# Kernel optimization log

Hardware: AMD Instinct MI355X
Metric: run time of the kernel (lower is better)

## Reference

```python
import jax, jax.numpy as jnp
import numpy as np

T, F, D = 16, 16, 512      # n_textures, n_features, texture resolution
N, L, H, W = 4, 4, 512, 512  # batch, n_layers, render H, render W


def setup_inputs() -> dict:
    key = jax.random.key(0)
    k1, k2, k3 = jax.random.split(key, 3)
    # grid_sample expects normalized coords in [-1, 1]
    uv_inputs = jax.random.uniform(k1, (N, 2 * L, H, W), jnp.float32) * 2.0 - 1.0
    mask_inputs = jax.random.randint(k2, (N, L, H, W), 0, T).astype(jnp.int32)
    data = jax.random.normal(k3, (T, F, D, D), jnp.float32) * 0.1
    return {"uv_inputs": uv_inputs, "mask_inputs": mask_inputs, "data": data}


def _sample_layer(data_flat, tid, u, v):
    # data_flat: [T*D*D, F]; tid,u,v: [N,H,W]
    # Faithful to torch grid_sample(bilinear, padding_mode='border', align_corners=False):
    # summing sample(data[t]) * (mask==t) over t == per-pixel gather from texture tid.
    ix = jnp.clip((u + 1.0) * (D * 0.5) - 0.5, 0.0, D - 1.0)  # border clip
    iy = jnp.clip((v + 1.0) * (D * 0.5) - 0.5, 0.0, D - 1.0)
    x0f = jnp.floor(ix)
    y0f = jnp.floor(iy)
    wx = (ix - x0f)[..., None]
    wy = (iy - y0f)[..., None]
    x0 = x0f.astype(jnp.int32)
    y0 = y0f.astype(jnp.int32)
    x1 = jnp.minimum(x0 + 1, D - 1)
    y1 = jnp.minimum(y0 + 1, D - 1)
    valid = ((tid >= 0) & (tid < T))[..., None]
    base = jnp.clip(tid, 0, T - 1).astype(jnp.int32) * (D * D)

    def g(y, x):  # gather corner texels -> [N,H,W,F]
        return jnp.take(data_flat, base + y * D + x, axis=0)

    out = (g(y0, x0) * (1.0 - wx) * (1.0 - wy)
           + g(y0, x1) * wx * (1.0 - wy)
           + g(y1, x0) * (1.0 - wx) * wy
           + g(y1, x1) * wx * wy)
    return out * valid.astype(out.dtype)


def reference(uv_inputs, mask_inputs, data):
    # [T,F,D,D] -> [T*D*D, F] so a single flat index gathers a full texel
    data_flat = jnp.transpose(data, (0, 2, 3, 1)).reshape(T * D * D, F)
    layers = []
    for l in range(L):  # small fixed layer count
        u = uv_inputs[:, 2 * l]       # grid[...,0] = x
        v = uv_inputs[:, 2 * l + 1]   # grid[...,1] = y
        tid = mask_inputs[:, l]
        sampled = _sample_layer(data_flat, tid, u, v)  # [N,H,W,F]
        layers.append(jnp.transpose(sampled, (0, 3, 1, 2)))  # [N,F,H,W]
    return jnp.concatenate(layers, axis=1)  # [N, L*F, H, W]
```

## Files before the change

kernel.cpp:

```cpp
#include <hip/hip_runtime.h>

constexpr int T_ = 16, F_ = 16, D_ = 512;
constexpr int N_ = 4, L_ = 4, H_ = 512, W_ = 512;
constexpr int HW_ = H_ * W_;
constexpr size_t DATA_ELEMS = (size_t)T_ * F_ * D_ * D_;
constexpr size_t PLANE = (size_t)D_ * D_;

constexpr size_t QTAB_BYTES = (size_t)T_ * D_ * D_ * 64;

__device__ unsigned g_smax_bits[T_ * F_];

typedef float vfloat4 __attribute__((ext_vector_type(4)));
typedef unsigned int vuint4 __attribute__((ext_vector_type(4)));

__global__ void zero_smax_kernel() { g_smax_bits[threadIdx.x] = 0u; }

__global__ __launch_bounds__(256) void max_pass_kernel(
    const float* __restrict__ data)
{
    const vfloat4* p = (const vfloat4*)data + (size_t)blockIdx.x * 8192 + threadIdx.x;
    float m = 0.0f;
    #pragma unroll
    for (int i = 0; i < 32; ++i) {
        vfloat4 v = __builtin_nontemporal_load(p + i * 256);
        m = fmaxf(m, fmaxf(fmaxf(fabsf(v.x), fabsf(v.y)),
                           fmaxf(fabsf(v.z), fabsf(v.w))));
    }
    #pragma unroll
    for (int k = 1; k < 64; k <<= 1) m = fmaxf(m, __shfl_xor(m, k));
    if ((threadIdx.x & 63) == 0)
        atomicMax(&g_smax_bits[blockIdx.x >> 3], __float_as_uint(m));
}

__global__ __launch_bounds__(256) void quad_pack_kernel(
    const float*   __restrict__ data,
    unsigned char* __restrict__ qtab)
{
    int bid = (blockIdx.x & 7) * 2048 + (blockIdx.x >> 3);

    __shared__ float enc[F_];
    int tid = threadIdx.x;
    int qblock = bid * 256;
    int t = qblock >> 18;
    if (tid < F_) {
        float m = __uint_as_float(g_smax_bits[t * F_ + tid]);
        enc[tid] = (m > 0.0f) ? 127.0f / m : 0.0f;
    }
    __syncthreads();

    int lane = tid & 63;
    int wid  = tid >> 6;
    int qbase = qblock + wid * 64;
    int dx = lane & 1, dy = (lane >> 1) & 1;
    int q0 = qbase + (lane >> 2);

    const float* dbase = data + (size_t)t * F_ * PLANE;
    unsigned out[4][4] = {};
    #pragma unroll
    for (int k = 0; k < 4; ++k) {
        int q = q0 + 16 * k;
        int x = q & (D_ - 1), y = (q >> 9) & (D_ - 1);
        int sx = min(x + dx, D_ - 1);
        int sy = min(y + dy, D_ - 1);
        size_t off = (size_t)sy * D_ + sx;
        #pragma unroll
        for (int f = 0; f < F_; ++f) {
            float val = dbase[f * PLANE + off];
            int i8 = __float2int_rn(fminf(fmaxf(val * enc[f], -127.0f), 127.0f));
            out[k][f >> 2] |= ((unsigned)i8 & 0xFFu) << (8 * (f & 3));
        }
    }
    unsigned char* wbase = qtab + (size_t)qbase * 64;
    #pragma unroll
    for (int k = 0; k < 4; ++k)
        *(vuint4*)(wbase + (size_t)(lane + 64 * k) * 16) =
            (vuint4){out[k][0], out[k][1], out[k][2], out[k][3]};
}

__global__ __launch_bounds__(256) void tex_sample_quad_kernel(
    const float*         __restrict__ uv,
    const int*           __restrict__ mask,
    const unsigned char* __restrict__ qtab,
    float*               __restrict__ out)
{
    __shared__ float dec[T_ * F_];
    dec[threadIdx.x] = __uint_as_float(g_smax_bits[threadIdx.x]) * (1.0f / 127.0f);
    __syncthreads();

    int idx = blockIdx.x * blockDim.x + threadIdx.x;
    int w = idx & (W_ - 1);
    int h = (idx >> 9) & (H_ - 1);
    int l = (idx >> 18) & (L_ - 1);
    int n = idx >> 20;
    int hw = h * W_ + w;

    float u  = __builtin_nontemporal_load(uv   + ((size_t)(n * 2 * L_ + 2 * l)    ) * HW_ + hw);
    float v  = __builtin_nontemporal_load(uv   + ((size_t)(n * 2 * L_ + 2 * l + 1)) * HW_ + hw);
    int  tid = __builtin_nontemporal_load(mask + ((size_t)(n * L_ + l)) * HW_ + hw);

    float ix = fminf(fmaxf((u + 1.0f) * (D_ * 0.5f) - 0.5f, 0.0f), (float)(D_ - 1));
    float iy = fminf(fmaxf((v + 1.0f) * (D_ * 0.5f) - 0.5f, 0.0f), (float)(D_ - 1));
    float x0f = floorf(ix), y0f = floorf(iy);
    float wx = ix - x0f, wy = iy - y0f;
    int x0 = (int)x0f, y0 = (int)y0f;

    float valid = (tid >= 0 && tid < T_) ? 1.0f : 0.0f;
    int t = min(max(tid, 0), T_ - 1);

    float w00 = (1.0f - wx) * (1.0f - wy) * valid;
    float w01 = wx * (1.0f - wy) * valid;
    float w10 = (1.0f - wx) * wy * valid;
    float w11 = wx * wy * valid;

    size_t e = ((size_t)t * D_ + y0) * D_ + x0;
    const vuint4* ep = (const vuint4*)(qtab + e * 64);
    vuint4 A = ep[0];
    vuint4 B = ep[1];
    vuint4 C = ep[2];
    vuint4 Dq = ep[3];

    const float* dp = &dec[t * F_];
    float* obase = out + ((size_t)(n * L_ + l) * F_) * HW_ + hw;
    #pragma unroll
    for (int q = 0; q < 4; ++q) {
        unsigned a = A[q], b = B[q], c = C[q], d = Dq[q];
        #pragma unroll
        for (int k = 0; k < 4; ++k) {
            int f = 4 * q + k;
            float r = (float)((signed char)(a >> (8 * k))) * w00
                    + (float)((signed char)(b >> (8 * k))) * w01
                    + (float)((signed char)(c >> (8 * k))) * w10
                    + (float)((signed char)(d >> (8 * k))) * w11;
            __builtin_nontemporal_store(r * dp[f], obase + (size_t)f * HW_);
        }
    }
}

__global__ __launch_bounds__(256) void tex_sample_kernel(
    const float* __restrict__ uv,
    const int*   __restrict__ mask,
    const float* __restrict__ data,
    float*       __restrict__ out)
{
    int idx = blockIdx.x * blockDim.x + threadIdx.x;
    int w = idx & (W_ - 1);
    int h = (idx >> 9) & (H_ - 1);
    int l = (idx >> 18) & (L_ - 1);
    int n = idx >> 20;
    int hw = h * W_ + w;

    float u  = uv[((size_t)(n * 2 * L_ + 2 * l)     ) * HW_ + hw];
    float v  = uv[((size_t)(n * 2 * L_ + 2 * l + 1)) * HW_ + hw];
    int  tid = mask[((size_t)(n * L_ + l)) * HW_ + hw];

    float ix = fminf(fmaxf((u + 1.0f) * (D_ * 0.5f) - 0.5f, 0.0f), (float)(D_ - 1));
    float iy = fminf(fmaxf((v + 1.0f) * (D_ * 0.5f) - 0.5f, 0.0f), (float)(D_ - 1));
    float x0f = floorf(ix), y0f = floorf(iy);
    float wx = ix - x0f, wy = iy - y0f;
    int x0 = (int)x0f, y0 = (int)y0f;
    int x1 = min(x0 + 1, D_ - 1);
    int y1 = min(y0 + 1, D_ - 1);

    float valid = (tid >= 0 && tid < T_) ? 1.0f : 0.0f;
    int t = min(max(tid, 0), T_ - 1);

    float w00 = (1.0f - wx) * (1.0f - wy) * valid;
    float w01 = wx * (1.0f - wy) * valid;
    float w10 = (1.0f - wx) * wy * valid;
    float w11 = wx * wy * valid;

    const float* dbase = data + (size_t)t * F_ * PLANE;
    int r0 = y0 * D_;
    int r1 = y1 * D_;
    float* obase = out + ((size_t)(n * L_ + l) * F_) * HW_ + hw;

    #pragma unroll
    for (int f = 0; f < F_; ++f) {
        const float* dp = dbase + (size_t)f * PLANE;
        float v00 = dp[r0 + x0];
        float v01 = dp[r0 + x1];
        float v10 = dp[r1 + x0];
        float v11 = dp[r1 + x1];
        obase[(size_t)f * HW_] = v00 * w00 + v01 * w01 + v10 * w10 + v11 * w11;
    }
}

extern "C" void kernel_launch(void* const* d_in, const int* in_sizes, int n_in,
                              void* d_out, int out_size, void* d_ws, size_t ws_size,
                              hipStream_t stream) {
    const float* uv   = (const float*)d_in[0];
    const int*   mask = (const int*)d_in[1];
    const float* data = (const float*)d_in[2];
    float* out = (float*)d_out;

    int total = N_ * L_ * H_ * W_;

    if (ws_size >= QTAB_BYTES) {
        unsigned char* qtab = (unsigned char*)d_ws;
        zero_smax_kernel<<<1, T_ * F_, 0, stream>>>();
        max_pass_kernel<<<2048, 256, 0, stream>>>(data);
        quad_pack_kernel<<<T_ * D_ * D_ / 256, 256, 0, stream>>>(data, qtab);
        tex_sample_quad_kernel<<<total / 256, 256, 0, stream>>>(uv, mask, qtab, out);
    } else {
        tex_sample_kernel<<<total / 256, 256, 0, stream>>>(uv, mask, data, out);
    }
}
```

Baseline: 748.1 us.

## Stage quantized texture rows in LDS to build quad table with coalesced loads

The quad-packing pre-pass now loads whole texture rows with coalesced float4 loads, quantizes them to int8 into shared memory (4 rows plus a halo row per block), then assembles the 2x2 neighbour quads from LDS. The old version loaded each texel four times with scattered scalar loads. The table layout also changes so each 16-byte group holds the four corners of one feature instead of one corner across four features, and the sampler is adjusted to match. The costs are about 41KB of LDS per block, which limits occupancy, and dropping the explicit clamp before rounding.

New measurement: 648.7 us. 13.3% less time.

```diff
diff --git a/kernel.cpp b/kernel.cpp
--- a/kernel.cpp
+++ b/kernel.cpp
@@ -32,49 +32,72 @@
         atomicMax(&g_smax_bits[blockIdx.x >> 3], __float_as_uint(m));
 }
 
-__global__ __launch_bounds__(256) void quad_pack_kernel(
+constexpr int QROWS = 4;
+constexpr int IROWS = QROWS + 1;
+constexpr int LDSP  = 520;
+
+__global__ __launch_bounds__(256) void quad_pack_kernel_v2(
     const float*   __restrict__ data,
     unsigned char* __restrict__ qtab)
 {
-    int bid = (blockIdx.x & 7) * 2048 + (blockIdx.x >> 3);
-
     __shared__ float enc[F_];
+    __shared__ unsigned char q8[F_][IROWS][LDSP];
+
+    int bid = blockIdx.x;
+    int t   = bid >> 7;
+    int yg  = bid & 127;
+    int y0  = yg * QROWS;
     int tid = threadIdx.x;
-    int qblock = bid * 256;
-    int t = qblock >> 18;
+
     if (tid < F_) {
         float m = __uint_as_float(g_smax_bits[t * F_ + tid]);
         enc[tid] = (m > 0.0f) ? 127.0f / m : 0.0f;
     }
     __syncthreads();
 
-    int lane = tid & 63;
-    int wid  = tid >> 6;
-    int qbase = qblock + wid * 64;
-    int dx = lane & 1, dy = (lane >> 1) & 1;
-    int q0 = qbase + (lane >> 2);
-
     const float* dbase = data + (size_t)t * F_ * PLANE;
-    unsigned out[4][4] = {};
-    #pragma unroll
-    for (int k = 0; k < 4; ++k) {
-        int q = q0 + 16 * k;
-        int x = q & (D_ - 1), y = (q >> 9) & (D_ - 1);
-        int sx = min(x + dx, D_ - 1);
-        int sy = min(y + dy, D_ - 1);
-        size_t off = (size_t)sy * D_ + sx;
+    #pragma unroll
+    for (int i = 0; i < IROWS; ++i) {
+        int ry = min(y0 + i, D_ - 1);
         #pragma unroll
-        for (int f = 0; f < F_; ++f) {
-            float val = dbase[f * PLANE + off];
-            int i8 = __float2int_rn(fminf(fmaxf(val * enc[f], -127.0f), 127.0f));
-            out[k][f >> 2] |= ((unsigned)i8 & 0xFFu) << (8 * (f & 3));
+        for (int j = 0; j < 8; ++j) {
+            int chunk = j * 256 + tid;
+            int f  = chunk >> 7;
+            int xq = chunk & 127;
+            vfloat4 v = __builtin_nontemporal_load(
+                (const vfloat4*)(dbase + (size_t)f * PLANE + (size_t)ry * D_) + xq);
+            float e = enc[f];
+            unsigned r;
+            r  = (unsigned)(__float2int_rn(v.x * e) & 0xFF);
+            r |= (unsigned)(__float2int_rn(v.y * e) & 0xFF) << 8;
+            r |= (unsigned)(__float2int_rn(v.z * e) & 0xFF) << 16;
+            r |= (unsigned)(__float2int_rn(v.w * e) & 0xFF) << 24;
+            *(unsigned*)&q8[f][i][4 * xq] = r;
         }
     }
-    unsigned char* wbase = qtab + (size_t)qbase * 64;
-    #pragma unroll
-    for (int k = 0; k < 4; ++k)
-        *(vuint4*)(wbase + (size_t)(lane + 64 * k) * 16) =
-            (vuint4){out[k][0], out[k][1], out[k][2], out[k][3]};
+    __syncthreads();
+
+    unsigned char* obase = qtab + ((size_t)t * D_ + y0) * D_ * 64;
+    #pragma unroll 8
+    for (int it = 0; it < 32; ++it) {
+        int chunk = it * 256 + tid;
+        int j  = chunk & 3;
+        int q  = chunk >> 2;
+        int ry = q >> 9;
+        int x  = q & (D_ - 1);
+        int x1 = min(x + 1, D_ - 1);
+        unsigned pk[4];
+        #pragma unroll
+        for (int ff = 0; ff < 4; ++ff) {
+            int f = 4 * j + ff;
+            unsigned b00 = q8[f][ry    ][x];
+            unsigned b01 = q8[f][ry    ][x1];
+            unsigned b10 = q8[f][ry + 1][x];
+            unsigned b11 = q8[f][ry + 1][x1];
+            pk[ff] = b00 | (b01 << 8) | (b10 << 16) | (b11 << 24);
+        }
+        *(vuint4*)(obase + (size_t)chunk * 16) = (vuint4){pk[0], pk[1], pk[2], pk[3]};
+    }
 }
 
 __global__ __launch_bounds__(256) void tex_sample_quad_kernel(
@@ -114,23 +137,24 @@
 
     size_t e = ((size_t)t * D_ + y0) * D_ + x0;
     const vuint4* ep = (const vuint4*)(qtab + e * 64);
-    vuint4 A = ep[0];
-    vuint4 B = ep[1];
-    vuint4 C = ep[2];
-    vuint4 Dq = ep[3];
+    vuint4 Q0 = ep[0];
+    vuint4 Q1 = ep[1];
+    vuint4 Q2 = ep[2];
+    vuint4 Q3 = ep[3];
 
     const float* dp = &dec[t * F_];
     float* obase = out + ((size_t)(n * L_ + l) * F_) * HW_ + hw;
     #pragma unroll
-    for (int q = 0; q < 4; ++q) {
-        unsigned a = A[q], b = B[q], c = C[q], d = Dq[q];
+    for (int qi = 0; qi < 4; ++qi) {
+        vuint4 G = (qi == 0) ? Q0 : (qi == 1) ? Q1 : (qi == 2) ? Q2 : Q3;
         #pragma unroll
         for (int k = 0; k < 4; ++k) {
-            int f = 4 * q + k;
-            float r = (float)((signed char)(a >> (8 * k))) * w00
-                    + (float)((signed char)(b >> (8 * k))) * w01
-                    + (float)((signed char)(c >> (8 * k))) * w10
-                    + (float)((signed char)(d >> (8 * k))) * w11;
+            int f = 4 * qi + k;
+            unsigned g = G[k];
+            float r = (float)((signed char)(g      )) * w00
+                    + (float)((signed char)(g >>  8)) * w01
+                    + (float)((signed char)(g >> 16)) * w10
+                    + (float)((signed char)(g >> 24)) * w11;
             __builtin_nontemporal_store(r * dp[f], obase + (size_t)f * HW_);
         }
     }
@@ -199,7 +223,7 @@
         unsigned char* qtab = (unsigned char*)d_ws;
         zero_smax_kernel<<<1, T_ * F_, 0, stream>>>();
         max_pass_kernel<<<2048, 256, 0, stream>>>(data);
-        quad_pack_kernel<<<T_ * D_ * D_ / 256, 256, 0, stream>>>(data, qtab);
+        quad_pack_kernel_v2<<<T_ * (D_ / QROWS), 256, 0, stream>>>(data, qtab);
         tex_sample_quad_kernel<<<total / 256, 256, 0, stream>>>(uv, mask, qtab, out);
     } else {
         tex_sample_kernel<<<total / 256, 256, 0, stream>>>(uv, mask, data, out);
```
